# Kernel optimization log

Measured on AMD Instinct MI355X. Metric: run time of the kernel, lower is better.

## Reference

```python
import jax, jax.numpy as jnp
import numpy as np

E = 768      # embed_dim (hidden_size)
H = 12       # num_attention_heads
DH = E // H  # head_dim = 64
B, S = 8, 1024


def setup_inputs() -> dict:
    key = jax.random.key(0)
    ks = jax.random.split(key, 10)
    sc = 1.0 / np.sqrt(E)
    inp = {
        "hidden_state": jax.random.normal(ks[0], (B, S, E), dtype=jnp.float32),
        # per-head Q/K/V projections, stacked over heads: [H, E, DH]
        "Wq": jax.random.normal(ks[1], (H, E, DH), dtype=jnp.float32) * sc,
        "bq": jax.random.normal(ks[2], (H, DH), dtype=jnp.float32) * 0.02,
        "Wk": jax.random.normal(ks[3], (H, E, DH), dtype=jnp.float32) * sc,
        "bk": jax.random.normal(ks[4], (H, DH), dtype=jnp.float32) * 0.02,
        "Wv": jax.random.normal(ks[5], (H, E, DH), dtype=jnp.float32) * sc,
        "bv": jax.random.normal(ks[6], (H, DH), dtype=jnp.float32) * 0.02,
        # output projection: [E, E]
        "Wo": jax.random.normal(ks[7], (E, E), dtype=jnp.float32) * sc,
        "bo": jax.random.normal(ks[8], (E,), dtype=jnp.float32) * 0.02,
    }
    return inp


def reference(hidden_state, Wq, bq, Wk, bk, Wv, bv, Wo, bo):
    # Q/K/V per head: [B,S,E] x [H,E,D] -> [B,H,S,D]
    q = jnp.einsum("bse,hed->bhsd", hidden_state, Wq) + bq[None, :, None, :]
    k = jnp.einsum("bse,hed->bhsd", hidden_state, Wk) + bk[None, :, None, :]
    v = jnp.einsum("bse,hed->bhsd", hidden_state, Wv) + bv[None, :, None, :]
    scale = 1.0 / jnp.sqrt(jnp.asarray(DH, dtype=q.dtype))
    scores = jnp.einsum("bhsd,bhtd->bhst", q, k) * scale   # [B,H,S,S]
    weights = jax.nn.softmax(scores, axis=-1)
    attn = jnp.einsum("bhst,bhtd->bhsd", weights, v)        # [B,H,S,D]
    # concat heads (head order matches ModuleList concat): [B,S,H*D]=[B,S,E]
    x = attn.transpose(0, 2, 1, 3).reshape(hidden_state.shape[0], hidden_state.shape[1], E)
    return x @ Wo + bo
```

## Files before the change

kernel.cpp:

```cpp
#include <hip/hip_runtime.h>

typedef unsigned short u16;
typedef __bf16 bf16;
typedef bf16 bf16x8 __attribute__((ext_vector_type(8)));
typedef float f32x4 __attribute__((ext_vector_type(4)));
typedef u16 u16x4 __attribute__((ext_vector_type(4)));
typedef u16 u16x8 __attribute__((ext_vector_type(8)));

#define MROWS 8192
#define EDIM 768
#define NQKV 2304
#define NHEAD 12
#define DH 64
#define SEQ 1024
#define BATCH 8
#define BH 96
#define BHSD (BH * SEQ * DH)
#define KIT64 (EDIM / 64)

#if __has_builtin(__builtin_amdgcn_exp2f)
#define EXP2(x) __builtin_amdgcn_exp2f(x)
#else
#define EXP2(x) exp2f(x)
#endif

__device__ __forceinline__ u16 f2bf(float f) {
  bf16 b = (bf16)f;
  return __builtin_bit_cast(u16, b);
}

__device__ __forceinline__ void gload_lds16(const u16* g, u16* l) {
  __builtin_amdgcn_global_load_lds(
      (const __attribute__((address_space(1))) void*)g,
      (__attribute__((address_space(3))) void*)l, 16, 0, 0);
}


__global__ void cvt_x(const float* __restrict__ x, u16* __restrict__ xb, int n) {
  int i = (blockIdx.x * blockDim.x + threadIdx.x) * 4;
  if (i >= n) return;
  float4 v = *(const float4*)(x + i);
  u16x4 o;
  o[0] = f2bf(v.x); o[1] = f2bf(v.y); o[2] = f2bf(v.z); o[3] = f2bf(v.w);
  *(u16x4*)(xb + i) = o;
}

__global__ __launch_bounds__(256) void pack_w(
    const float* __restrict__ Wq, const float* __restrict__ Wk,
    const float* __restrict__ Wv, const float* __restrict__ Wo,
    u16* __restrict__ Wt, u16* __restrict__ Wot) {
  __shared__ float T[64][65];
  int bid = blockIdx.x;
  int tid = threadIdx.x;
  int c = tid & 63, r4 = tid >> 6;
  if (bid < 432) {
    int region = bid / 144, rem = bid - region * 144;
    int h = rem / 12, e0 = (rem - h * 12) * 64;
    const float* W = region == 0 ? Wq : (region == 1 ? Wk : Wv);
    for (int p = 0; p < 16; p++) {
      int er = r4 + p * 4;
      T[er][c] = W[(size_t)(h * EDIM + e0 + er) * DH + c];
    }
    __syncthreads();
    int nbase = region * EDIM + h * 64;
    for (int p = 0; p < 16; p++) {
      int dr = r4 + p * 4;
      Wt[(size_t)(nbase + dr) * EDIM + e0 + c] = f2bf(T[c][dr]);
    }
  } else {
    bid -= 432;
    int n0 = (bid / 12) * 64, e0 = (bid - (bid / 12) * 12) * 64;
    for (int p = 0; p < 16; p++) {
      int er = r4 + p * 4;
      T[er][c] = Wo[(size_t)(e0 + er) * EDIM + n0 + c];
    }
    __syncthreads();
    for (int p = 0; p < 16; p++) {
      int dr = r4 + p * 4;
      Wot[(size_t)(n0 + dr) * EDIM + e0 + c] = f2bf(T[c][dr]);
    }
  }
}

__device__ __forceinline__ void gemm_core64(
    const u16* __restrict__ A, const u16* __restrict__ Bt,
    u16* As, u16* Bs,
    int m0, int n0, int tid, f32x4 acc[4][4]) {
  int wv = __builtin_amdgcn_readfirstlane(tid >> 6);
  int lane = tid & 63, quad = lane >> 4, l16 = lane & 15;
  int wm = (wv & 1) * 64, wn = (wv >> 1) * 64;
  int lr = lane >> 3, cpos = lane & 7;
  int swcol = (cpos ^ lr) * 8;
  const u16* Ag = A + (size_t)(m0 + wv * 32 + lr) * EDIM + swcol;
  const u16* Bg = Bt + (size_t)(n0 + wv * 32 + lr) * EDIM + swcol;
  u16* Asl = As + (wv * 32 + lr) * 64 + cpos * 8;
  u16* Bsl = Bs + (wv * 32 + lr) * 64 + cpos * 8;

  for (int k = 0; k < KIT64; k++) {
    __syncthreads();
    const u16* ak = Ag + k * 64;
    const u16* bk = Bg + k * 64;
#pragma unroll
    for (int q = 0; q < 4; q++) {
      gload_lds16(ak + q * 8 * EDIM, Asl + q * 512);
      gload_lds16(bk + q * 8 * EDIM, Bsl + q * 512);
    }
    __syncthreads();
#pragma unroll
    for (int kh = 0; kh < 2; kh++) {
      bf16x8 af[4], bfr[4];
      for (int i = 0; i < 4; i++) {
        int row = wm + i * 16 + l16;
        af[i] = *(const bf16x8*)(As + row * 64 + (((kh * 4 + quad) ^ (row & 7))) * 8);
      }
      for (int j = 0; j < 4; j++) {
        int row = wn + j * 16 + l16;
        bfr[j] = *(const bf16x8*)(Bs + row * 64 + (((kh * 4 + quad) ^ (row & 7))) * 8);
      }
      for (int i = 0; i < 4; i++)
        for (int j = 0; j < 4; j++)
          acc[i][j] = __builtin_amdgcn_mfma_f32_16x16x32_bf16(af[i], bfr[j], acc[i][j], 0, 0, 0);
    }
  }
}

__global__ __launch_bounds__(256, 4) void gemm_qkv(
    const u16* __restrict__ A, const u16* __restrict__ Bt,
    const float* __restrict__ bq, const float* __restrict__ bk, const float* __restrict__ bv,
    u16* __restrict__ qkv) {
  __shared__ __align__(16) u16 As[128 * 64];
  __shared__ __align__(16) u16 Bs[128 * 64];
  int tid = threadIdx.x;
  int wv = tid >> 6, lane = tid & 63, quad = lane >> 4, l16 = lane & 15;
  int wm = (wv & 1) * 64, wn = (wv >> 1) * 64;
  int lin = blockIdx.y * 64 + blockIdx.x;
  int xcd = lin & 7, r8 = lin >> 3;
  int m0 = (xcd * 8 + (r8 & 7)) * 128;
  int n0 = (r8 >> 3) * 128;
  f32x4 acc[4][4] = {};
  gemm_core64(A, Bt, As, Bs, m0, n0, tid, acc);

  const float kQscale = 0.18033688011112042f;
  for (int i = 0; i < 4; i++) {
    int row0 = m0 + wm + i * 16 + quad * 4;
    for (int j = 0; j < 4; j++) {
      int n = n0 + wn + j * 16 + l16;
      int region = n / EDIM;
      int hd = n - region * EDIM;
      int h = hd >> 6, d = hd & 63;
      const float* bp = region == 0 ? bq : (region == 1 ? bk : bv);
      float bias = bp[hd];
      float scale = region == 0 ? kQscale : 1.0f;
      for (int r = 0; r < 4; r++) {
        int rr = row0 + r;
        int bb = rr >> 10, s = rr & 1023;
        float val = (acc[i][j][r] + bias) * scale;
        u16 bv16 = f2bf(val);
        int bhh = bb * NHEAD + h;
        if (region < 2) {
          qkv[(size_t)region * BHSD + ((size_t)bhh * SEQ + s) * DH + d] = bv16;
        } else {
          qkv[(size_t)2 * BHSD + ((size_t)bhh * DH + d) * SEQ + s] = bv16;
        }
      }
    }
  }
}

__global__ __launch_bounds__(256, 4) void attn_kernel(const u16* __restrict__ qkv, u16* __restrict__ attn) {
  int lin = blockIdx.y * 96 + blockIdx.x;
  int xcd = lin & 7, rr6 = lin >> 3;
  int bh = xcd * 12 + (rr6 >> 4);
  int qt = rr6 & 15;
  int b = bh / NHEAD, h = bh - b * NHEAD;
  const u16* Q  = qkv + (size_t)bh * SEQ * DH;
  const u16* K  = qkv + (size_t)(BH + bh) * SEQ * DH;
  const u16* VT = qkv + (size_t)(2 * BH + bh) * SEQ * DH;
  int tid = threadIdx.x, wave = tid >> 6, lane = tid & 63, quad = lane >> 4, l16 = lane & 15;
  int q_base = qt * 64 + wave * 16;

  __shared__ u16 Ks[64 * 64];
  __shared__ u16 Vts[64 * 64];
  __shared__ u16 Ps[4][16 * 64];

  bf16x8 qf[2];
  for (int c = 0; c < 2; c++)
    qf[c] = *(const bf16x8*)(Q + (size_t)(q_base + l16) * DH + c * 32 + quad * 8);

  f32x4 o[4] = {};
  float psum[4] = {};

  int tr = tid >> 3, cpos = tid & 7;
  int ssw = (cpos ^ (tr & 7)) * 8;
  u16* KsW0 = Ks + tr * 64 + ssw;
  u16* KsW1 = Ks + (tr + 32) * 64 + ssw;
  u16* VsW0 = Vts + tr * 64 + ssw;
  u16* VsW1 = Vts + (tr + 32) * 64 + ssw;
  int tc8 = cpos * 8;

  u16x8 kv0 = *(const u16x8*)(K + (size_t)tr * DH + tc8);
  u16x8 kv1 = *(const u16x8*)(K + (size_t)(32 + tr) * DH + tc8);
  u16x8 vv0 = *(const u16x8*)(VT + (size_t)tr * SEQ + tc8);
  u16x8 vv1 = *(const u16x8*)(VT + (size_t)(32 + tr) * SEQ + tc8);

  for (int t0 = 0; t0 < SEQ; t0 += 64) {
    __syncthreads();
    *(u16x8*)KsW0 = kv0;
    *(u16x8*)KsW1 = kv1;
    *(u16x8*)VsW0 = vv0;
    *(u16x8*)VsW1 = vv1;
    __syncthreads();
    if (t0 + 64 < SEQ) {
      kv0 = *(const u16x8*)(K + (size_t)(t0 + 64 + tr) * DH + tc8);
      kv1 = *(const u16x8*)(K + (size_t)(t0 + 96 + tr) * DH + tc8);
      vv0 = *(const u16x8*)(VT + (size_t)tr * SEQ + t0 + 64 + tc8);
      vv1 = *(const u16x8*)(VT + (size_t)(32 + tr) * SEQ + t0 + 64 + tc8);
    }

    float p[4][4];
    for (int tc = 0; tc < 4; tc++) {
      int krow = tc * 16 + l16, k7 = l16 & 7;
      bf16x8 kf0 = *(const bf16x8*)(Ks + krow * 64 + ((quad ^ k7) * 8));
      bf16x8 kf1 = *(const bf16x8*)(Ks + krow * 64 + (((4 + quad) ^ k7) * 8));
      f32x4 z = {};
      z = __builtin_amdgcn_mfma_f32_16x16x32_bf16(qf[0], kf0, z, 0, 0, 0);
      z = __builtin_amdgcn_mfma_f32_16x16x32_bf16(qf[1], kf1, z, 0, 0, 0);
      for (int r = 0; r < 4; r++) {
        p[tc][r] = EXP2(z[r]);
        psum[r] += p[tc][r];
      }
    }

    u16* P = Ps[wave];
    for (int tc = 0; tc < 4; tc++)
      for (int r = 0; r < 4; r++) {
        int prow = quad * 4 + r;
        int pc = tc * 2 + (l16 >> 3);
        P[prow * 64 + ((pc ^ (prow & 7)) * 8) + (l16 & 7)] = f2bf(p[tc][r]);
      }
    bf16x8 pf[2];
    for (int kc = 0; kc < 2; kc++)
      pf[kc] = *(const bf16x8*)(Ps[wave] + l16 * 64 + (((kc * 4 + quad) ^ (l16 & 7)) * 8));

    for (int n = 0; n < 4; n++) {
      int vrow = n * 16 + l16, v7 = l16 & 7;
      bf16x8 vf0 = *(const bf16x8*)(Vts + vrow * 64 + ((quad ^ v7) * 8));
      bf16x8 vf1 = *(const bf16x8*)(Vts + vrow * 64 + (((4 + quad) ^ v7) * 8));
      o[n] = __builtin_amdgcn_mfma_f32_16x16x32_bf16(pf[0], vf0, o[n], 0, 0, 0);
      o[n] = __builtin_amdgcn_mfma_f32_16x16x32_bf16(pf[1], vf1, o[n], 0, 0, 0);
    }
  }

  for (int m = 1; m < 16; m <<= 1)
    for (int r = 0; r < 4; r++)
      psum[r] += __shfl_xor(psum[r], m);

  for (int r = 0; r < 4; r++) {
    float inv = 1.0f / psum[r];
    int qrow = q_base + quad * 4 + r;
    size_t rowoff = (size_t)(b * SEQ + qrow) * EDIM + h * DH;
    for (int n = 0; n < 4; n++)
      attn[rowoff + n * 16 + l16] = f2bf(o[n][r] * inv);
  }
}

__global__ __launch_bounds__(256, 4) void gemm_out(
    const u16* __restrict__ A, const u16* __restrict__ Bt,
    const float* __restrict__ bo, float* __restrict__ out) {
  __shared__ __align__(16) u16 As[128 * 64];
  __shared__ __align__(16) u16 Bs[128 * 64];
  int tid = threadIdx.x;
  int wv = tid >> 6, lane = tid & 63, quad = lane >> 4, l16 = lane & 15;
  int wm = (wv & 1) * 64, wn = (wv >> 1) * 64;
  int lin = blockIdx.y * 64 + blockIdx.x;
  int xcd = lin & 7, r8 = lin >> 3;
  int m0 = (xcd * 8 + (r8 & 7)) * 128;
  int n0 = (r8 >> 3) * 128;
  f32x4 acc[4][4] = {};
  gemm_core64(A, Bt, As, Bs, m0, n0, tid, acc);

  for (int i = 0; i < 4; i++) {
    int row0 = m0 + wm + i * 16 + quad * 4;
    for (int j = 0; j < 4; j++) {
      int n = n0 + wn + j * 16 + l16;
      float bias = bo[n];
      for (int r = 0; r < 4; r++)
        out[(size_t)(row0 + r) * EDIM + n] = acc[i][j][r] + bias;
    }
  }
}

extern "C" void kernel_launch(void* const* d_in, const int* in_sizes, int n_in,
                              void* d_out, int out_size, void* d_ws, size_t ws_size,
                              hipStream_t stream) {
  const float* x  = (const float*)d_in[0];
  const float* Wq = (const float*)d_in[1];
  const float* bq = (const float*)d_in[2];
  const float* Wk = (const float*)d_in[3];
  const float* bk = (const float*)d_in[4];
  const float* Wv = (const float*)d_in[5];
  const float* bv = (const float*)d_in[6];
  const float* Wo = (const float*)d_in[7];
  const float* bo = (const float*)d_in[8];
  float* out = (float*)d_out;
  char* ws = (char*)d_ws;

  u16* Xb   = (u16*)(ws);
  u16* Wt   = (u16*)(ws + 12582912);
  u16* Wot  = (u16*)(ws + 16121856);
  u16* qkv  = (u16*)(ws + 17301504);
  u16* attn = (u16*)(ws + 55050240);

  cvt_x<<<6144, 256, 0, stream>>>(x, Xb, MROWS * EDIM);
  pack_w<<<576, 256, 0, stream>>>(Wq, Wk, Wv, Wo, Wt, Wot);
  gemm_qkv<<<dim3(64, 18), 256, 0, stream>>>(Xb, Wt, bq, bk, bv, qkv);
  attn_kernel<<<dim3(96, 16), 256, 0, stream>>>(qkv, attn);
  gemm_out<<<dim3(64, 6), 256, 0, stream>>>(attn, Wot, bo, out);
}
```

Baseline: 209.6 us.

## Double-buffer K/V tiles in attention with direct global-to-LDS loads

The attention kernel now stages K and V^T tiles into two LDS buffers using direct global-to-LDS loads (gload_lds16), prefetching the next tile while computing on the current one. This drops the register round-trip and one of the two barriers per iteration. It also raises wave priority around the MFMA sections with s_setprio. LDS use per block roughly doubles for K/V, which could cut occupancy at 4 blocks per CU. The swizzle moves from the LDS write side to the global read address.

Result: no change. 208.2 us (-0.7%).

```diff
diff --git a/kernel.cpp b/kernel.cpp
--- a/kernel.cpp
+++ b/kernel.cpp
@@ -179,9 +179,9 @@
   int tid = threadIdx.x, wave = tid >> 6, lane = tid & 63, quad = lane >> 4, l16 = lane & 15;
   int q_base = qt * 64 + wave * 16;
 
-  __shared__ u16 Ks[64 * 64];
-  __shared__ u16 Vts[64 * 64];
-  __shared__ u16 Ps[4][16 * 64];
+  __shared__ __align__(16) u16 Ks[2][64 * 64];
+  __shared__ __align__(16) u16 Vts[2][64 * 64];
+  __shared__ __align__(16) u16 Ps[4][16 * 64];
 
   bf16x8 qf[2];
   for (int c = 0; c < 2; c++)
@@ -192,36 +192,37 @@
 
   int tr = tid >> 3, cpos = tid & 7;
   int ssw = (cpos ^ (tr & 7)) * 8;
-  u16* KsW0 = Ks + tr * 64 + ssw;
-  u16* KsW1 = Ks + (tr + 32) * 64 + ssw;
-  u16* VsW0 = Vts + tr * 64 + ssw;
-  u16* VsW1 = Vts + (tr + 32) * 64 + ssw;
-  int tc8 = cpos * 8;
-
-  u16x8 kv0 = *(const u16x8*)(K + (size_t)tr * DH + tc8);
-  u16x8 kv1 = *(const u16x8*)(K + (size_t)(32 + tr) * DH + tc8);
-  u16x8 vv0 = *(const u16x8*)(VT + (size_t)tr * SEQ + tc8);
-  u16x8 vv1 = *(const u16x8*)(VT + (size_t)(32 + tr) * SEQ + tc8);
-
+  const u16* Kg0 = K + (size_t)tr * DH + ssw;
+  const u16* Kg1 = K + (size_t)(tr + 32) * DH + ssw;
+  const u16* Vg0 = VT + (size_t)tr * SEQ + ssw;
+  const u16* Vg1 = VT + (size_t)(tr + 32) * SEQ + ssw;
+  int dst0 = tr * 64 + cpos * 8;
+  int dst1 = (tr + 32) * 64 + cpos * 8;
+
+  gload_lds16(Kg0, Ks[0] + dst0);
+  gload_lds16(Kg1, Ks[0] + dst1);
+  gload_lds16(Vg0, Vts[0] + dst0);
+  gload_lds16(Vg1, Vts[0] + dst1);
+  __syncthreads();
+
+  int buf = 0;
   for (int t0 = 0; t0 < SEQ; t0 += 64) {
-    __syncthreads();
-    *(u16x8*)KsW0 = kv0;
-    *(u16x8*)KsW1 = kv1;
-    *(u16x8*)VsW0 = vv0;
-    *(u16x8*)VsW1 = vv1;
-    __syncthreads();
     if (t0 + 64 < SEQ) {
-      kv0 = *(const u16x8*)(K + (size_t)(t0 + 64 + tr) * DH + tc8);
-      kv1 = *(const u16x8*)(K + (size_t)(t0 + 96 + tr) * DH + tc8);
-      vv0 = *(const u16x8*)(VT + (size_t)tr * SEQ + t0 + 64 + tc8);
-      vv1 = *(const u16x8*)(VT + (size_t)(32 + tr) * SEQ + t0 + 64 + tc8);
-    }
+      int nb = buf ^ 1;
+      gload_lds16(Kg0 + (size_t)(t0 + 64) * DH, Ks[nb] + dst0);
+      gload_lds16(Kg1 + (size_t)(t0 + 64) * DH, Ks[nb] + dst1);
+      gload_lds16(Vg0 + t0 + 64, Vts[nb] + dst0);
+      gload_lds16(Vg1 + t0 + 64, Vts[nb] + dst1);
+    }
+    const u16* Kb = Ks[buf];
+    const u16* Vb = Vts[buf];
 
     float p[4][4];
+    __builtin_amdgcn_s_setprio(1);
     for (int tc = 0; tc < 4; tc++) {
       int krow = tc * 16 + l16, k7 = l16 & 7;
-      bf16x8 kf0 = *(const bf16x8*)(Ks + krow * 64 + ((quad ^ k7) * 8));
-      bf16x8 kf1 = *(const bf16x8*)(Ks + krow * 64 + (((4 + quad) ^ k7) * 8));
+      bf16x8 kf0 = *(const bf16x8*)(Kb + krow * 64 + ((quad ^ k7) * 8));
+      bf16x8 kf1 = *(const bf16x8*)(Kb + krow * 64 + (((4 + quad) ^ k7) * 8));
       f32x4 z = {};
       z = __builtin_amdgcn_mfma_f32_16x16x32_bf16(qf[0], kf0, z, 0, 0, 0);
       z = __builtin_amdgcn_mfma_f32_16x16x32_bf16(qf[1], kf1, z, 0, 0, 0);
@@ -230,6 +231,7 @@
         psum[r] += p[tc][r];
       }
     }
+    __builtin_amdgcn_s_setprio(0);
 
     u16* P = Ps[wave];
     for (int tc = 0; tc < 4; tc++)
@@ -242,13 +244,18 @@
     for (int kc = 0; kc < 2; kc++)
       pf[kc] = *(const bf16x8*)(Ps[wave] + l16 * 64 + (((kc * 4 + quad) ^ (l16 & 7)) * 8));
 
+    __builtin_amdgcn_s_setprio(1);
     for (int n = 0; n < 4; n++) {
       int vrow = n * 16 + l16, v7 = l16 & 7;
-      bf16x8 vf0 = *(const bf16x8*)(Vts + vrow * 64 + ((quad ^ v7) * 8));
-      bf16x8 vf1 = *(const bf16x8*)(Vts + vrow * 64 + (((4 + quad) ^ v7) * 8));
+      bf16x8 vf0 = *(const bf16x8*)(Vb + vrow * 64 + ((quad ^ v7) * 8));
+      bf16x8 vf1 = *(const bf16x8*)(Vb + vrow * 64 + (((4 + quad) ^ v7) * 8));
       o[n] = __builtin_amdgcn_mfma_f32_16x16x32_bf16(pf[0], vf0, o[n], 0, 0, 0);
       o[n] = __builtin_amdgcn_mfma_f32_16x16x32_bf16(pf[1], vf1, o[n], 0, 0, 0);
     }
+    __builtin_amdgcn_s_setprio(0);
+
+    __syncthreads();
+    buf ^= 1;
   }
 
   for (int m = 1; m < 16; m <<= 1)
```
